# Performance work log

Measured on AMD Instinct MI355X. Metric: run time of the kernel, lower is better.

## Reference

```python
import jax, jax.numpy as jnp
import numpy as np

TIME_STEPS = 100
MIN_LATENCY = 0
MAX_LATENCY = 99
THRESHOLD = 0.5
NOISE_STD = 0.01


def setup_inputs() -> dict:
    key = jax.random.key(0)
    k1, k2 = jax.random.split(key)
    x = jax.random.normal(k1, (256, 4096), dtype=jnp.float32)
    noise = jax.random.normal(k2, (256, 4096), dtype=jnp.float32)
    return {"x": x, "noise": noise}


def reference(x, noise):
    # x, noise: [B, F]
    x_noisy = x + noise * NOISE_STD
    x_norm = jax.nn.sigmoid(x_noisy)
    latencies = MIN_LATENCY + (1.0 - x_norm) * (MAX_LATENCY - MIN_LATENCY)
    latencies = jnp.clip(jnp.round(latencies).astype(jnp.int32), MIN_LATENCY, MAX_LATENCY)
    should_spike = x_norm > THRESHOLD                      # [B, F] bool
    # vectorized one-hot scatter: spikes[b, f, latencies[b, f]] = 1 if should_spike
    one_hot = jax.nn.one_hot(latencies, TIME_STEPS, dtype=jnp.float32)  # [B, F, T]
    spikes = one_hot * should_spike[..., None].astype(jnp.float32)
    return spikes
```

## Files before the change

kernel.cpp:

```cpp
#include <hip/hip_runtime.h>


#define TIME_STEPS 100
#define PAIRS_PER_BLOCK 256
#define F4_PER_PAIR (TIME_STEPS / 4)
#define F4_PER_THREAD (PAIRS_PER_BLOCK * F4_PER_PAIR / 256)

typedef float vf4 __attribute__((ext_vector_type(4)));

__global__ __launch_bounds__(256) void latency_encode_kernel(
    const float* __restrict__ x, const float* __restrict__ noise,
    float* __restrict__ out, int npairs) {
  __shared__ int lat_s[PAIRS_PER_BLOCK];

  const int tid = threadIdx.x;
  const int pairBase = blockIdx.x * PAIRS_PER_BLOCK;
  const int p = pairBase + tid;

  int lat = -1;
  if (p < npairs) {
    double xn = (double)x[p] + (double)noise[p] * 0.01;
    double s = 1.0 / (1.0 + exp(-xn));
    int li = (int)rint((1.0 - s) * 99.0);
    li = li < 0 ? 0 : (li > 99 ? 99 : li);
    lat = (s > 0.5) ? li : -1;
  }
  lat_s[tid] = lat;
  __syncthreads();

  vf4* o4 = (vf4*)(out + (size_t)pairBase * TIME_STEPS);
#pragma unroll
  for (int k = 0; k < F4_PER_THREAD; ++k) {
    const int fi4 = tid + k * 256;
    const int pl = fi4 / F4_PER_PAIR;
    const int pos = (fi4 % F4_PER_PAIR) * 4;
    const int L = lat_s[pl];
    vf4 v;
    v.x = (L == pos + 0) ? 1.0f : 0.0f;
    v.y = (L == pos + 1) ? 1.0f : 0.0f;
    v.z = (L == pos + 2) ? 1.0f : 0.0f;
    v.w = (L == pos + 3) ? 1.0f : 0.0f;
    if (pairBase + pl < npairs) __builtin_nontemporal_store(v, &o4[fi4]);
  }
}

extern "C" void kernel_launch(void* const* d_in, const int* in_sizes, int n_in,
                              void* d_out, int out_size, void* d_ws, size_t ws_size,
                              hipStream_t stream) {
  const float* x = (const float*)d_in[0];
  const float* noise = (const float*)d_in[1];
  float* out = (float*)d_out;
  const int npairs = in_sizes[0];
  const int grid = (npairs + PAIRS_PER_BLOCK - 1) / PAIRS_PER_BLOCK;
  latency_encode_kernel<<<grid, 256, 0, stream>>>(x, noise, out, npairs);
}
```

Baseline: 85.42 us.

## Process four chunks per block with double-buffered latency prefetch

Each block now handles four 256-pair chunks instead of one. While writing the one-hot output for the current chunk, it loads inputs for the next chunk, then computes that chunk's latencies into a second shared buffer. The aim is to overlap the input loads and double-precision sigmoid with the output stores and to cut block launch overhead. It also drops the nontemporal store hint in favour of plain stores, which may change how the large write stream interacts with the cache. The grid is four times smaller, which lowers parallelism for a kernel bound by write bandwidth.

New measurement: 88.14 us. +3.2%, slower.

```diff
diff --git a/kernel.cpp b/kernel.cpp
--- a/kernel.cpp
+++ b/kernel.cpp
@@ -1,46 +1,73 @@
 #include <hip/hip_runtime.h>
 
 
-#define TIME_STEPS 100
-#define PAIRS_PER_BLOCK 256
-#define F4_PER_PAIR (TIME_STEPS / 4)
-#define F4_PER_THREAD (PAIRS_PER_BLOCK * F4_PER_PAIR / 256)
+#define T 100
+#define PPC 256
+#define CPB 4
 
 typedef float vf4 __attribute__((ext_vector_type(4)));
+
+__device__ __forceinline__ int pair_latency(float xv, float nv) {
+  double xn = (double)xv + (double)nv * 0.01;
+  double s = 1.0 / (1.0 + exp(-xn));
+  int li = (int)rint((1.0 - s) * 99.0);
+  li = li < 0 ? 0 : (li > 99 ? 99 : li);
+  return (s > 0.5) ? li : -1;
+}
 
 __global__ __launch_bounds__(256) void latency_encode_kernel(
     const float* __restrict__ x, const float* __restrict__ noise,
     float* __restrict__ out, int npairs) {
-  __shared__ int lat_s[PAIRS_PER_BLOCK];
+  __shared__ int lat_s[2][PPC];
 
   const int tid = threadIdx.x;
-  const int pairBase = blockIdx.x * PAIRS_PER_BLOCK;
-  const int p = pairBase + tid;
+  const long long chunk0 = (long long)blockIdx.x * CPB;
+  const long long nchunks = (npairs + PPC - 1) / PPC;
 
-  int lat = -1;
-  if (p < npairs) {
-    double xn = (double)x[p] + (double)noise[p] * 0.01;
-    double s = 1.0 / (1.0 + exp(-xn));
-    int li = (int)rint((1.0 - s) * 99.0);
-    li = li < 0 ? 0 : (li > 99 ? 99 : li);
-    lat = (s > 0.5) ? li : -1;
+  {
+    const long long p = chunk0 * PPC + tid;
+    int lat = -1;
+    if (chunk0 < nchunks && p < npairs) lat = pair_latency(x[p], noise[p]);
+    lat_s[0][tid] = lat;
   }
-  lat_s[tid] = lat;
   __syncthreads();
 
-  vf4* o4 = (vf4*)(out + (size_t)pairBase * TIME_STEPS);
+  int buf = 0;
 #pragma unroll
-  for (int k = 0; k < F4_PER_THREAD; ++k) {
-    const int fi4 = tid + k * 256;
-    const int pl = fi4 / F4_PER_PAIR;
-    const int pos = (fi4 % F4_PER_PAIR) * 4;
-    const int L = lat_s[pl];
-    vf4 v;
-    v.x = (L == pos + 0) ? 1.0f : 0.0f;
-    v.y = (L == pos + 1) ? 1.0f : 0.0f;
-    v.z = (L == pos + 2) ? 1.0f : 0.0f;
-    v.w = (L == pos + 3) ? 1.0f : 0.0f;
-    if (pairBase + pl < npairs) __builtin_nontemporal_store(v, &o4[fi4]);
+  for (int k = 0; k < CPB; ++k) {
+    const long long c = chunk0 + k;
+    if (c >= nchunks) break;
+
+    float xv2 = 0.f, nv2 = 0.f;
+    bool haveNext = (k + 1 < CPB) && (c + 1 < nchunks);
+    if (haveNext) {
+      const long long pn = (c + 1) * PPC + tid;
+      if (pn < npairs) { xv2 = x[pn]; nv2 = noise[pn]; }
+    }
+
+    vf4* __restrict__ o4 = (vf4*)(out + c * PPC * (long long)T);
+    const bool full = (c + 1) * PPC <= npairs;
+    const long long lim4 = full ? 6400 : (npairs - c * PPC) * T / 4;
+#pragma unroll
+    for (int j = 0; j < 25; ++j) {
+      const int fi4 = tid + j * 256;
+      const int pl = fi4 / 25;
+      const int pos = (fi4 % 25) * 4;
+      const int L = lat_s[buf][pl];
+      vf4 v;
+      v.x = (L == pos + 0) ? 1.0f : 0.0f;
+      v.y = (L == pos + 1) ? 1.0f : 0.0f;
+      v.z = (L == pos + 2) ? 1.0f : 0.0f;
+      v.w = (L == pos + 3) ? 1.0f : 0.0f;
+      if (full || fi4 < lim4) o4[fi4] = v;
+    }
+
+    if (haveNext) {
+      const long long pn = (c + 1) * PPC + tid;
+      lat_s[buf ^ 1][tid] = (pn < npairs) ? pair_latency(xv2, nv2) : -1;
+      __syncthreads();
+      buf ^= 1;
+    }
   }
 }
 
@@ -51,6 +78,7 @@
   const float* noise = (const float*)d_in[1];
   float* out = (float*)d_out;
   const int npairs = in_sizes[0];
-  const int grid = (npairs + PAIRS_PER_BLOCK - 1) / PAIRS_PER_BLOCK;
+  const long long nchunks = (npairs + PPC - 1) / PPC;
+  const int grid = (int)((nchunks + CPB - 1) / CPB);
   latency_encode_kernel<<<grid, 256, 0, stream>>>(x, noise, out, npairs);
 }
```

## Split latency encoding into byte-latency pass and grid-stride one-hot streaming kernel

Applied to the files above, without the earlier changes.

Latencies are now computed by a separate kernel into a one-byte-per-pair workspace buffer. A second grid-stride kernel with a fixed grid then streams the 400MB-scale one-hot output using plain (not nontemporal) stores, reading each latency from that buffer. The fused kernel is kept as a fallback for when the workspace is too small. The aim is to decouple the fp64 sigmoid work from the write stream and use a persistent-style launch. In exchange it adds a second launch and an extra global round trip for the latencies, and it drops the nontemporal store hint.

Result: faster. 80.45 us, median of 2 (-5.8%).

```diff
diff --git a/kernel.cpp b/kernel.cpp
--- a/kernel.cpp
+++ b/kernel.cpp
@@ -1,46 +1,66 @@
 #include <hip/hip_runtime.h>
 
 
-#define TIME_STEPS 100
-#define PAIRS_PER_BLOCK 256
-#define F4_PER_PAIR (TIME_STEPS / 4)
-#define F4_PER_THREAD (PAIRS_PER_BLOCK * F4_PER_PAIR / 256)
+#define T 100
 
 typedef float vf4 __attribute__((ext_vector_type(4)));
 
-__global__ __launch_bounds__(256) void latency_encode_kernel(
+__device__ __forceinline__ int pair_latency_f64(float xv, float nv) {
+  double xn = (double)xv + (double)nv * 0.01;
+  double s = 1.0 / (1.0 + exp(-xn));
+  int li = (int)rint((1.0 - s) * 99.0);
+  li = li < 0 ? 0 : (li > 99 ? 99 : li);
+  return (s > 0.5) ? li : 255;
+}
+
+__global__ __launch_bounds__(256) void lat_kernel(
+    const float* __restrict__ x, const float* __restrict__ noise,
+    unsigned char* __restrict__ lat, int npairs) {
+  const int stride = gridDim.x * 256;
+  for (int p = blockIdx.x * 256 + threadIdx.x; p < npairs; p += stride)
+    lat[p] = (unsigned char)pair_latency_f64(x[p], noise[p]);
+}
+
+__global__ __launch_bounds__(256) void onehot_stream_kernel(
+    const unsigned char* __restrict__ lat, vf4* __restrict__ o4, int n4) {
+  const int stride = gridDim.x * 256;
+  for (int i = blockIdx.x * 256 + threadIdx.x; i < n4; i += stride) {
+    const int pair = i / 25;
+    const int pos = (i - pair * 25) * 4;
+    const int L = lat[pair];
+    vf4 v;
+    v.x = (L == pos + 0) ? 1.0f : 0.0f;
+    v.y = (L == pos + 1) ? 1.0f : 0.0f;
+    v.z = (L == pos + 2) ? 1.0f : 0.0f;
+    v.w = (L == pos + 3) ? 1.0f : 0.0f;
+    o4[i] = v;
+  }
+}
+
+__global__ __launch_bounds__(256) void latency_encode_fused(
     const float* __restrict__ x, const float* __restrict__ noise,
     float* __restrict__ out, int npairs) {
-  __shared__ int lat_s[PAIRS_PER_BLOCK];
-
+  __shared__ int lat_s[256];
   const int tid = threadIdx.x;
-  const int pairBase = blockIdx.x * PAIRS_PER_BLOCK;
+  const int pairBase = blockIdx.x * 256;
   const int p = pairBase + tid;
-
-  int lat = -1;
-  if (p < npairs) {
-    double xn = (double)x[p] + (double)noise[p] * 0.01;
-    double s = 1.0 / (1.0 + exp(-xn));
-    int li = (int)rint((1.0 - s) * 99.0);
-    li = li < 0 ? 0 : (li > 99 ? 99 : li);
-    lat = (s > 0.5) ? li : -1;
-  }
+  int lat = 255;
+  if (p < npairs) lat = pair_latency_f64(x[p], noise[p]);
   lat_s[tid] = lat;
   __syncthreads();
-
-  vf4* o4 = (vf4*)(out + (size_t)pairBase * TIME_STEPS);
+  vf4* o4 = (vf4*)(out + (size_t)pairBase * T);
 #pragma unroll
-  for (int k = 0; k < F4_PER_THREAD; ++k) {
+  for (int k = 0; k < 25; ++k) {
     const int fi4 = tid + k * 256;
-    const int pl = fi4 / F4_PER_PAIR;
-    const int pos = (fi4 % F4_PER_PAIR) * 4;
+    const int pl = fi4 / 25;
+    const int pos = (fi4 % 25) * 4;
     const int L = lat_s[pl];
     vf4 v;
     v.x = (L == pos + 0) ? 1.0f : 0.0f;
     v.y = (L == pos + 1) ? 1.0f : 0.0f;
     v.z = (L == pos + 2) ? 1.0f : 0.0f;
     v.w = (L == pos + 3) ? 1.0f : 0.0f;
-    if (pairBase + pl < npairs) __builtin_nontemporal_store(v, &o4[fi4]);
+    if (pairBase + pl < npairs) o4[fi4] = v;
   }
 }
 
@@ -51,6 +71,14 @@
   const float* noise = (const float*)d_in[1];
   float* out = (float*)d_out;
   const int npairs = in_sizes[0];
-  const int grid = (npairs + PAIRS_PER_BLOCK - 1) / PAIRS_PER_BLOCK;
-  latency_encode_kernel<<<grid, 256, 0, stream>>>(x, noise, out, npairs);
+
+  if (ws_size >= (size_t)npairs) {
+    unsigned char* lat = (unsigned char*)d_ws;
+    lat_kernel<<<1024, 256, 0, stream>>>(x, noise, lat, npairs);
+    const int n4 = out_size / 4;
+    onehot_stream_kernel<<<2048, 256, 0, stream>>>(lat, (vf4*)out, n4);
+  } else {
+    const int grid = (npairs + 255) / 256;
+    latency_encode_fused<<<grid, 256, 0, stream>>>(x, noise, out, npairs);
+  }
 }
```
